# Kernel optimization log

Measured on AMD Instinct MI355X. Metric: run time of the kernel, lower is better.

Reference implementation:

```python
import jax, jax.numpy as jnp
from jax import lax
import numpy as np

D_MODEL = 256
EXPAND = 2
D_INNER = D_MODEL * EXPAND
B, T = 8, 4096


def setup_inputs() -> dict:
    key = jax.random.key(0)
    ks = jax.random.split(key, 7)
    s_lin = 1.0 / np.sqrt(D_MODEL)
    s_gru_i = 1.0 / np.sqrt(D_MODEL)  # torch GRU init: U(-1/sqrt(hidden), 1/sqrt(hidden))
    x = jax.random.normal(ks[0], (B, T, D_MODEL), dtype=jnp.float32)
    W1 = jax.random.uniform(ks[1], (D_INNER, D_MODEL), jnp.float32, -s_lin, s_lin)
    b1 = jax.random.uniform(ks[2], (D_INNER,), jnp.float32, -s_lin, s_lin)
    W_ih = jax.random.uniform(ks[3], (3 * D_MODEL, D_INNER), jnp.float32, -s_gru_i, s_gru_i)
    b_ih = jax.random.uniform(ks[4], (3 * D_MODEL,), jnp.float32, -s_gru_i, s_gru_i)
    W_hh = jax.random.uniform(ks[5], (3 * D_MODEL, D_MODEL), jnp.float32, -s_gru_i, s_gru_i)
    b_hh = jax.random.uniform(ks[6], (3 * D_MODEL,), jnp.float32, -s_gru_i, s_gru_i)
    return {"x": x, "W1": W1, "b1": b1, "W_ih": W_ih, "b_ih": b_ih, "W_hh": W_hh, "b_hh": b_hh}


def reference(x, W1, b1, W_ih, b_ih, W_hh, b_hh):
    # Linear(d_model -> d_inner) + exact GELU (torch default)
    h = jax.nn.gelu(jnp.einsum('btd,id->bti', x, W1) + b1, approximate=False)  # [B,T,Di]
    Bb, Tt, _ = h.shape
    H = W_hh.shape[1]
    # Precompute input-side gate pre-activations for all timesteps (order: r, z, n)
    gx = jnp.einsum('bti,gi->btg', h, W_ih) + b_ih  # [B,T,3H]
    gx = jnp.moveaxis(gx, 1, 0)                     # [T,B,3H]

    def step(hprev, g):
        gh = hprev @ W_hh.T + b_hh                  # [B,3H]
        xr, xz, xn = jnp.split(g, 3, axis=-1)
        hr, hz, hn = jnp.split(gh, 3, axis=-1)
        r = jax.nn.sigmoid(xr + hr)
        z = jax.nn.sigmoid(xz + hz)
        n = jnp.tanh(xn + r * hn)
        hnew = (1.0 - z) * n + z * hprev
        return hnew, hnew

    h0 = jnp.zeros((Bb, H), dtype=x.dtype)
    _, out = lax.scan(step, h0, gx)                 # out: [T,B,H]
    return jnp.moveaxis(out, 0, 1)                  # [B,T,H]
```

## Files before the change

kernel.cpp:

```cpp
#include <hip/hip_runtime.h>
#include <hip/hip_fp16.h>

#define DM   256
#define DI   512
#define TG   768
#define TSEQ 4096
#define NB   8
#define MTOT (NB*TSEQ)

typedef _Float16 f16x4 __attribute__((ext_vector_type(4)));
typedef _Float16 f16x8 __attribute__((ext_vector_type(8)));
typedef float    f32x4 __attribute__((ext_vector_type(4)));

template<bool A_HALF, bool GELU_ACT, bool TNB_OUT>
__global__ __launch_bounds__(256) void gemm_bias(
    const void* __restrict__ Ap, const float* __restrict__ W,
    const float* __restrict__ bias, __half* __restrict__ C,
    int M, int N, int K)
{
  __shared__ float As[16][132];
  __shared__ float Ws[16][132];
  const int tid = threadIdx.x;
  const int tx = tid & 15, ty = tid >> 4;
  const int m0 = blockIdx.y * 128;
  const int n0 = blockIdx.x * 128;

  float acc[8][8] = {};

  for (int k0 = 0; k0 < K; k0 += 16) {
    if constexpr (A_HALF) {
      const __half* A = (const __half*)Ap;
      int r = tid >> 1, seg = (tid & 1) * 8;
      float4 raw = *(const float4*)(A + (size_t)(m0 + r) * K + k0 + seg);
      const __half* hv = (const __half*)&raw;
      #pragma unroll
      for (int q = 0; q < 8; q++) As[seg + q][r] = __half2float(hv[q]);
    } else {
      const float* A = (const float*)Ap;
      #pragma unroll
      for (int rep = 0; rep < 2; rep++) {
        int r = (tid >> 2) + rep * 64;
        int seg = (tid & 3) * 4;
        float4 v = *(const float4*)(A + (size_t)(m0 + r) * K + k0 + seg);
        As[seg + 0][r] = v.x; As[seg + 1][r] = v.y;
        As[seg + 2][r] = v.z; As[seg + 3][r] = v.w;
      }
    }
    #pragma unroll
    for (int rep = 0; rep < 2; rep++) {
      int r = (tid >> 2) + rep * 64;
      int seg = (tid & 3) * 4;
      float4 v = *(const float4*)(W + (size_t)(n0 + r) * K + k0 + seg);
      Ws[seg + 0][r] = v.x; Ws[seg + 1][r] = v.y;
      Ws[seg + 2][r] = v.z; Ws[seg + 3][r] = v.w;
    }
    __syncthreads();
    #pragma unroll
    for (int kk = 0; kk < 16; ++kk) {
      float a[8], b[8];
      *(float4*)&a[0] = *(const float4*)&As[kk][ty * 8];
      *(float4*)&a[4] = *(const float4*)&As[kk][ty * 8 + 4];
      *(float4*)&b[0] = *(const float4*)&Ws[kk][tx * 8];
      *(float4*)&b[4] = *(const float4*)&Ws[kk][tx * 8 + 4];
      #pragma unroll
      for (int i = 0; i < 8; i++)
        #pragma unroll
        for (int j = 0; j < 8; j++)
          acc[i][j] += a[i] * b[j];
    }
    __syncthreads();
  }

  #pragma unroll
  for (int i = 0; i < 8; i++) {
    int m = m0 + ty * 8 + i;
    #pragma unroll
    for (int j = 0; j < 8; j++) {
      int n = n0 + tx * 8 + j;
      float v = acc[i][j] + bias[n];
      if constexpr (GELU_ACT) {
        v = 0.5f * v * (1.0f + erff(v * 0.70710678118654752f));
      }
      if constexpr (TNB_OUT) {
        C[((size_t)(m & (TSEQ - 1)) * TG + n) * NB + (m >> 12)] = __float2half(v);
      } else {
        C[(size_t)m * N + n] = __float2half(v);
      }
    }
  }
}

#define MFMA16(A, B, C) __builtin_amdgcn_mfma_f32_16x16x32_f16(A, B, C, 0, 0, 0)

#define LDB(NM, G, C, KT) f16x8 NM; { \
    const float* p_ = Whh + (size_t)(256*(G) + 16*((C)*8 + w) + col) * DM + (KT)*32 + kgrp*8; \
    float4 fa_ = *(const float4*)p_; float4 fb_ = *(const float4*)(p_ + 4);    \
    NM[0]=(_Float16)fa_.x; NM[1]=(_Float16)fa_.y; NM[2]=(_Float16)fa_.z; NM[3]=(_Float16)fa_.w; \
    NM[4]=(_Float16)fb_.x; NM[5]=(_Float16)fb_.y; NM[6]=(_Float16)fb_.z; NM[7]=(_Float16)fb_.w; }

#define LDB8(P, G, C) \
  LDB(P##0, G, C, 0) LDB(P##1, G, C, 1) LDB(P##2, G, C, 2) LDB(P##3, G, C, 3) \
  LDB(P##4, G, C, 4) LDB(P##5, G, C, 5) LDB(P##6, G, C, 6) LDB(P##7, G, C, 7)

#define MSTEP(RA, ZA, NA, BR, BZ, BN, KT) {                                    \
    f16x8 a_ = *(const f16x8*)&hb[cur][col][(KT)*32 + kgrp*8];                 \
    RA = MFMA16(a_, BR, RA); ZA = MFMA16(a_, BZ, ZA); NA = MFMA16(a_, BN, NA); }

__device__ __forceinline__ float selswap(float x, float y, int lane) {
  float ys = __shfl(y, lane ^ 32, 64);
  return (lane < 32) ? x : ys;
}

__global__ __attribute__((amdgpu_flat_work_group_size(512, 512)))
__attribute__((amdgpu_waves_per_eu(2, 2)))
void gru_scan(
    const __half* __restrict__ gxb,
    const float*  __restrict__ Whh,
    const float*  __restrict__ bhh,
    float* __restrict__ out)
{
  const int tid  = threadIdx.x;
  const int w    = tid >> 6;
  const int lane = tid & 63;
  const int col  = lane & 15;
  const int kgrp = lane >> 4;
  const int ch   = lane >> 5;
  const int bb   = ((lane >> 4) & 1) * 4;

  __shared__ __align__(16) _Float16 hb[2][16][264];

  for (int i = tid; i < 2 * 16 * 264; i += 512) ((_Float16*)hb)[i] = (_Float16)0.0f;

  LDB8(bR0, 0, 0) LDB8(bZ0, 1, 0) LDB8(bN0, 2, 0)
  LDB8(bR1, 0, 1) LDB8(bZ1, 1, 1) LDB8(bN1, 2, 1)

  const int u = 16 * (w + 8 * ch) + col;
  const float brv = bhh[u];
  const float bzv = bhh[DM + u];
  const float bnv = bhh[2 * DM + u];
  float hl0 = 0.f, hl1 = 0.f, hl2 = 0.f, hl3 = 0.f;

  __syncthreads();

  const __half* gp = gxb + (size_t)u * NB + bb;
  f16x4 gr_c = *(const f16x4*)(gp);
  f16x4 gz_c = *(const f16x4*)(gp + 2048);
  f16x4 gn_c = *(const f16x4*)(gp + 4096);

  for (int t = 0; t < TSEQ; ++t) {
    const int cur = t & 1, nxt = cur ^ 1;

    const __half* gq = gp + ((t < TSEQ - 1) ? TG * NB : 0);
    f16x4 gr_n = *(const f16x4*)(gq);
    f16x4 gz_n = *(const f16x4*)(gq + 2048);
    f16x4 gn_n = *(const f16x4*)(gq + 4096);

    const f32x4 Zv = {0.f, 0.f, 0.f, 0.f};
    f32x4 R0 = Zv, Z0 = Zv, N0 = Zv;
    MSTEP(R0, Z0, N0, bR00, bZ00, bN00, 0) MSTEP(R0, Z0, N0, bR01, bZ01, bN01, 1)
    MSTEP(R0, Z0, N0, bR02, bZ02, bN02, 2) MSTEP(R0, Z0, N0, bR03, bZ03, bN03, 3)
    MSTEP(R0, Z0, N0, bR04, bZ04, bN04, 4) MSTEP(R0, Z0, N0, bR05, bZ05, bN05, 5)
    MSTEP(R0, Z0, N0, bR06, bZ06, bN06, 6) MSTEP(R0, Z0, N0, bR07, bZ07, bN07, 7)
    f32x4 R1 = Zv, Z1 = Zv, N1 = Zv;
    MSTEP(R1, Z1, N1, bR10, bZ10, bN10, 0) MSTEP(R1, Z1, N1, bR11, bZ11, bN11, 1)
    MSTEP(R1, Z1, N1, bR12, bZ12, bN12, 2) MSTEP(R1, Z1, N1, bR13, bZ13, bN13, 3)
    MSTEP(R1, Z1, N1, bR14, bZ14, bN14, 4) MSTEP(R1, Z1, N1, bR15, bZ15, bN15, 5)
    MSTEP(R1, Z1, N1, bR16, bZ16, bN16, 6) MSTEP(R1, Z1, N1, bR17, bZ17, bN17, 7)

    #define GATE(i, HL) {                                                      \
      float ghr = selswap(R0[i], R1[i], lane);                                 \
      float ghz = selswap(Z0[i], Z1[i], lane);                                 \
      float ghn = selswap(N0[i], N1[i], lane);                                 \
      float xr = (float)gr_c[i], xz = (float)gz_c[i], xn = (float)gn_c[i];     \
      float rg = __builtin_amdgcn_rcpf(1.0f + __expf(-(xr + ghr + brv)));      \
      float zg = __builtin_amdgcn_rcpf(1.0f + __expf(-(xz + ghz + bzv)));      \
      float ap = xn + rg * (ghn + bnv);                                        \
      float e  = __expf(-2.0f * __builtin_fabsf(ap));                          \
      float nn = __builtin_copysignf(                                          \
          (1.0f - e) * __builtin_amdgcn_rcpf(1.0f + e), ap);                   \
      float hnew = nn + zg * (HL - nn);                                        \
      HL = hnew;                                                               \
      hb[nxt][bb + (i)][u] = (_Float16)hnew;                                   \
      out[((size_t)(bb + (i)) * TSEQ + t) * DM + u] = hnew;                    \
    }
    GATE(0, hl0) GATE(1, hl1) GATE(2, hl2) GATE(3, hl3)
    #undef GATE

    __syncthreads();

    gp = gq;
    gr_c = gr_n; gz_c = gz_n; gn_c = gn_n;
  }
}

extern "C" void kernel_launch(void* const* d_in, const int* in_sizes, int n_in,
                              void* d_out, int out_size, void* d_ws, size_t ws_size,
                              hipStream_t stream) {
  const float* x   = (const float*)d_in[0];
  const float* W1  = (const float*)d_in[1];
  const float* b1  = (const float*)d_in[2];
  const float* Wih = (const float*)d_in[3];
  const float* bih = (const float*)d_in[4];
  const float* Whh = (const float*)d_in[5];
  const float* bhh = (const float*)d_in[6];
  float* out = (float*)d_out;

  char* ws = (char*)d_ws;
  __half* h  = (__half*)ws;
  size_t h_bytes = (size_t)MTOT * DI * sizeof(__half);
  h_bytes = (h_bytes + 255) & ~(size_t)255;
  __half* gxbuf = (__half*)(ws + h_bytes);

  dim3 blk(256);
  gemm_bias<false, true, false><<<dim3(DI / 128, MTOT / 128), blk, 0, stream>>>(
      x, W1, b1, h, MTOT, DI, DM);
  gemm_bias<true, false, true><<<dim3(TG / 128, MTOT / 128), blk, 0, stream>>>(
      h, Wih, bih, gxbuf, MTOT, TG, DI);
  gru_scan<<<1, 512, 0, stream>>>(gxbuf, Whh, bhh, out);
}
```

Before: 6.062 ms.

## Stage GRU gate inputs via async global-to-LDS loads and spill W_hh tail to LDS

```diff
diff --git a/kernel.cpp b/kernel.cpp
--- a/kernel.cpp
+++ b/kernel.cpp
@@ -92,27 +92,33 @@
 
 #define MFMA16(A, B, C) __builtin_amdgcn_mfma_f32_16x16x32_f16(A, B, C, 0, 0, 0)
 
+__device__ __forceinline__ void gload_lds(const void* g, void* l) {
+  __builtin_amdgcn_global_load_lds(
+      (const __attribute__((address_space(1))) unsigned int*)g,
+      (__attribute__((address_space(3))) unsigned int*)l, 4, 0, 0);
+}
+
+__device__ __forceinline__ float selswap(float x, float y, int lane) {
+  float ys = __shfl(y, lane ^ 32, 64);
+  return (lane < 32) ? x : ys;
+}
+
 #define LDB(NM, G, C, KT) f16x8 NM; { \
     const float* p_ = Whh + (size_t)(256*(G) + 16*((C)*8 + w) + col) * DM + (KT)*32 + kgrp*8; \
     float4 fa_ = *(const float4*)p_; float4 fb_ = *(const float4*)(p_ + 4);    \
     NM[0]=(_Float16)fa_.x; NM[1]=(_Float16)fa_.y; NM[2]=(_Float16)fa_.z; NM[3]=(_Float16)fa_.w; \
     NM[4]=(_Float16)fb_.x; NM[5]=(_Float16)fb_.y; NM[6]=(_Float16)fb_.z; NM[7]=(_Float16)fb_.w; }
 
-#define LDB8(P, G, C) \
+#define LDB7(P, G, C) \
   LDB(P##0, G, C, 0) LDB(P##1, G, C, 1) LDB(P##2, G, C, 2) LDB(P##3, G, C, 3) \
-  LDB(P##4, G, C, 4) LDB(P##5, G, C, 5) LDB(P##6, G, C, 6) LDB(P##7, G, C, 7)
-
-#define MSTEP(RA, ZA, NA, BR, BZ, BN, KT) {                                    \
-    f16x8 a_ = *(const f16x8*)&hb[cur][col][(KT)*32 + kgrp*8];                 \
-    RA = MFMA16(a_, BR, RA); ZA = MFMA16(a_, BZ, ZA); NA = MFMA16(a_, BN, NA); }
-
-__device__ __forceinline__ float selswap(float x, float y, int lane) {
-  float ys = __shfl(y, lane ^ 32, 64);
-  return (lane < 32) ? x : ys;
-}
+  LDB(P##4, G, C, 4) LDB(P##5, G, C, 5) LDB(P##6, G, C, 6)
+
+#define KSTEP(KT, BR0, BZ0, BN0, BR1, BZ1, BN1) {                              \
+    f16x8 a_ = *(const f16x8*)(hp + (KT)*64);                                  \
+    R0 = MFMA16(a_, BR0, R0); Z0 = MFMA16(a_, BZ0, Z0); N0 = MFMA16(a_, BN0, N0); \
+    R1 = MFMA16(a_, BR1, R1); Z1 = MFMA16(a_, BZ1, Z1); N1 = MFMA16(a_, BN1, N1); }
 
 __global__ __attribute__((amdgpu_flat_work_group_size(512, 512)))
-__attribute__((amdgpu_waves_per_eu(2, 2)))
 void gru_scan(
     const __half* __restrict__ gxb,
     const float*  __restrict__ Whh,
@@ -127,12 +133,22 @@
   const int ch   = lane >> 5;
   const int bb   = ((lane >> 4) & 1) * 4;
 
-  __shared__ __align__(16) _Float16 hb[2][16][264];
-
-  for (int i = tid; i < 2 * 16 * 264; i += 512) ((_Float16*)hb)[i] = (_Float16)0.0f;
-
-  LDB8(bR0, 0, 0) LDB8(bZ0, 1, 0) LDB8(bN0, 2, 0)
-  LDB8(bR1, 0, 1) LDB8(bZ1, 1, 1) LDB8(bN1, 2, 1)
+  __shared__ __align__(16) _Float16 pool[49152];
+
+  for (int i = tid; i < 8448; i += 512) pool[i] = (_Float16)0.0f;
+  for (int idx = tid; idx < 768 * 32; idx += 512) {
+    int un = idx >> 5, k = idx & 31;
+    pool[20736 + un * 32 + k] = (_Float16)Whh[(size_t)un * DM + 224 + k];
+  }
+
+  LDB7(bR0_, 0, 0) LDB7(bZ0_, 1, 0) LDB7(bN0_, 2, 0)
+  LDB7(bR1_, 0, 1) LDB7(bZ1_, 1, 1) LDB7(bN1_, 2, 1)
+  asm volatile("" : "+a"(bR0_0), "+a"(bR0_1), "+a"(bR0_2), "+a"(bR0_3), "+a"(bR0_4), "+a"(bR0_5), "+a"(bR0_6));
+  asm volatile("" : "+a"(bZ0_0), "+a"(bZ0_1), "+a"(bZ0_2), "+a"(bZ0_3), "+a"(bZ0_4), "+a"(bZ0_5), "+a"(bZ0_6));
+  asm volatile("" : "+a"(bN0_0), "+a"(bN0_1), "+a"(bN0_2), "+a"(bN0_3), "+a"(bN0_4), "+a"(bN0_5), "+a"(bN0_6));
+  asm volatile("" : "+a"(bR1_0), "+a"(bR1_1), "+a"(bR1_2), "+a"(bR1_3), "+a"(bR1_4), "+a"(bR1_5), "+a"(bR1_6));
+  asm volatile("" : "+a"(bZ1_0), "+a"(bZ1_1), "+a"(bZ1_2), "+a"(bZ1_3), "+a"(bZ1_4), "+a"(bZ1_5), "+a"(bZ1_6));
+  asm volatile("" : "+a"(bN1_0), "+a"(bN1_1), "+a"(bN1_2), "+a"(bN1_3), "+a"(bN1_4), "+a"(bN1_5), "+a"(bN1_6));
 
   const int u = 16 * (w + 8 * ch) + col;
   const float brv = bhh[u];
@@ -140,56 +156,79 @@
   const float bnv = bhh[2 * DM + u];
   float hl0 = 0.f, hl1 = 0.f, hl2 = 0.f, hl3 = 0.f;
 
+  {
+    const __half* s = gxb + (size_t)w * 768 + lane * 2;
+    _Float16* d = &pool[8448 + w * 768];
+    gload_lds(s, d); gload_lds(s + 128, d + 128); gload_lds(s + 256, d + 256);
+    gload_lds(s + 384, d + 384); gload_lds(s + 512, d + 512); gload_lds(s + 640, d + 640);
+  }
   __syncthreads();
 
-  const __half* gp = gxb + (size_t)u * NB + bb;
-  f16x4 gr_c = *(const f16x4*)(gp);
-  f16x4 gz_c = *(const f16x4*)(gp + 2048);
-  f16x4 gn_c = *(const f16x4*)(gp + 4096);
+  const char* hbase  = (const char*)pool + col * 528 + kgrp * 16;
+  const char* gbase  = (const char*)pool + 16896 + u * 16 + bb * 2;
+  char*       hwbase = (char*)pool + bb * 528 + u * 2;
+  const char* wl     = (const char*)pool + 41472 + (16 * w + col) * 64 + kgrp * 16;
 
   for (int t = 0; t < TSEQ; ++t) {
     const int cur = t & 1, nxt = cur ^ 1;
 
-    const __half* gq = gp + ((t < TSEQ - 1) ? TG * NB : 0);
-    f16x4 gr_n = *(const f16x4*)(gq);
-    f16x4 gz_n = *(const f16x4*)(gq + 2048);
-    f16x4 gn_n = *(const f16x4*)(gq + 4096);
-
+    {
+      int ts = (t + 1 < TSEQ) ? t + 1 : t;
+      const __half* s = gxb + (size_t)ts * 6144 + w * 768 + lane * 2;
+      _Float16* d = &pool[8448 + nxt * 6144 + w * 768];
+      gload_lds(s, d); gload_lds(s + 128, d + 128); gload_lds(s + 256, d + 256);
+      gload_lds(s + 384, d + 384); gload_lds(s + 512, d + 512); gload_lds(s + 640, d + 640);
+    }
+
+    const char* hp = hbase + cur * 8448;
     const f32x4 Zv = {0.f, 0.f, 0.f, 0.f};
-    f32x4 R0 = Zv, Z0 = Zv, N0 = Zv;
-    MSTEP(R0, Z0, N0, bR00, bZ00, bN00, 0) MSTEP(R0, Z0, N0, bR01, bZ01, bN01, 1)
-    MSTEP(R0, Z0, N0, bR02, bZ02, bN02, 2) MSTEP(R0, Z0, N0, bR03, bZ03, bN03, 3)
-    MSTEP(R0, Z0, N0, bR04, bZ04, bN04, 4) MSTEP(R0, Z0, N0, bR05, bZ05, bN05, 5)
-    MSTEP(R0, Z0, N0, bR06, bZ06, bN06, 6) MSTEP(R0, Z0, N0, bR07, bZ07, bN07, 7)
-    f32x4 R1 = Zv, Z1 = Zv, N1 = Zv;
-    MSTEP(R1, Z1, N1, bR10, bZ10, bN10, 0) MSTEP(R1, Z1, N1, bR11, bZ11, bN11, 1)
-    MSTEP(R1, Z1, N1, bR12, bZ12, bN12, 2) MSTEP(R1, Z1, N1, bR13, bZ13, bN13, 3)
-    MSTEP(R1, Z1, N1, bR14, bZ14, bN14, 4) MSTEP(R1, Z1, N1, bR15, bZ15, bN15, 5)
-    MSTEP(R1, Z1, N1, bR16, bZ16, bN16, 6) MSTEP(R1, Z1, N1, bR17, bZ17, bN17, 7)
+    f32x4 R0 = Zv, Z0 = Zv, N0 = Zv, R1 = Zv, Z1 = Zv, N1 = Zv;
+    KSTEP(0, bR0_0, bZ0_0, bN0_0, bR1_0, bZ1_0, bN1_0)
+    KSTEP(1, bR0_1, bZ0_1, bN0_1, bR1_1, bZ1_1, bN1_1)
+    KSTEP(2, bR0_2, bZ0_2, bN0_2, bR1_2, bZ1_2, bN1_2)
+    KSTEP(3, bR0_3, bZ0_3, bN0_3, bR1_3, bZ1_3, bN1_3)
+    KSTEP(4, bR0_4, bZ0_4, bN0_4, bR1_4, bZ1_4, bN1_4)
+    KSTEP(5, bR0_5, bZ0_5, bN0_5, bR1_5, bZ1_5, bN1_5)
+    KSTEP(6, bR0_6, bZ0_6, bN0_6, bR1_6, bZ1_6, bN1_6)
+    {
+      f16x8 a_ = *(const f16x8*)(hp + 7 * 64);
+      f16x8 t0 = *(const f16x8*)(wl);
+      f16x8 t1 = *(const f16x8*)(wl + 8192);
+      R0 = MFMA16(a_, t0, R0); R1 = MFMA16(a_, t1, R1);
+      f16x8 t2 = *(const f16x8*)(wl + 16384);
+      f16x8 t3 = *(const f16x8*)(wl + 24576);
+      Z0 = MFMA16(a_, t2, Z0); Z1 = MFMA16(a_, t3, Z1);
+      f16x8 t4 = *(const f16x8*)(wl + 32768);
+      f16x8 t5 = *(const f16x8*)(wl + 40960);
+      N0 = MFMA16(a_, t4, N0); N1 = MFMA16(a_, t5, N1);
+    }
+
+    const char* gl = gbase + cur * 12288;
+    f16x4 gr4 = *(const f16x4*)(gl);
+    f16x4 gz4 = *(const f16x4*)(gl + 4096);
+    f16x4 gn4 = *(const f16x4*)(gl + 8192);
+    char* hw = hwbase + nxt * 8448;
 
     #define GATE(i, HL) {                                                      \
       float ghr = selswap(R0[i], R1[i], lane);                                 \
       float ghz = selswap(Z0[i], Z1[i], lane);                                 \
       float ghn = selswap(N0[i], N1[i], lane);                                 \
-      float xr = (float)gr_c[i], xz = (float)gz_c[i], xn = (float)gn_c[i];     \
+      float xr = (float)gr4[i], xz = (float)gz4[i], xn = (float)gn4[i];        \
       float rg = __builtin_amdgcn_rcpf(1.0f + __expf(-(xr + ghr + brv)));      \
       float zg = __builtin_amdgcn_rcpf(1.0f + __expf(-(xz + ghz + bzv)));      \
       float ap = xn + rg * (ghn + bnv);                                        \
       float e  = __expf(-2.0f * __builtin_fabsf(ap));                          \
-      float nn = __builtin_copysignf(                                          \
+      float nn2 = __builtin_copysignf(                                         \
           (1.0f - e) * __builtin_amdgcn_rcpf(1.0f + e), ap);                   \
-      float hnew = nn + zg * (HL - nn);                                        \
+      float hnew = nn2 + zg * (HL - nn2);                                      \
       HL = hnew;                                                               \
-      hb[nxt][bb + (i)][u] = (_Float16)hnew;                                   \
+      *(_Float16*)(hw + (i) * 528) = (_Float16)hnew;                           \
       out[((size_t)(bb + (i)) * TSEQ + t) * DM + u] = hnew;                    \
     }
     GATE(0, hl0) GATE(1, hl1) GATE(2, hl2) GATE(3, hl3)
     #undef GATE
 
     __syncthreads();
-
-    gp = gq;
-    gr_c = gr_n; gz_c = gz_n; gn_c = gn_n;
   }
 }
 
```

After: 7.595 ms. +25.3%, slower.
